# Kernel optimization log

Measured on AMD Instinct MI355X. Metric: run time of the kernel, lower is better.

## Reference

```python
import jax, jax.numpy as jnp
import numpy as np

HEAD_DIM = 128
NUM_HEADS = 16
GROUP_SIZE = 8


def setup_inputs() -> dict:
    key = jax.random.key(0)
    k1, k2, k3 = jax.random.split(key, 3)
    B, T, K = 2, 2048, 2048
    query = jax.random.normal(k1, (B, T, NUM_HEADS * HEAD_DIM), dtype=jnp.float32)
    k_ = jax.random.normal(k2, (B, K, NUM_HEADS, HEAD_DIM), dtype=jnp.float32)
    v_ = jax.random.normal(k3, (B, K, NUM_HEADS, HEAD_DIM), dtype=jnp.float32)
    return {"query": query, "key": k_, "value": v_}


def reference(query, key, value):
    B, T, _ = query.shape
    g = GROUP_SIZE
    # (B, T//g, g, H, D)
    gq = query.reshape(B, T // g, g, NUM_HEADS, HEAD_DIM)
    scale = jnp.sqrt(jnp.asarray(HEAD_DIM, dtype=query.dtype))
    # scores: (B, T//g, g, H, K)
    scores = jnp.einsum('btghd,bkhd->btghk', gq, key) / scale
    attention = jax.nn.softmax(scores, axis=-1)
    out = jnp.einsum('btghk,bkhd->btghd', attention, value)
    return out.reshape(B, T, -1)
```

## Files before the change

kernel.cpp:

```cpp
#include <hip/hip_runtime.h>


#define T_   2048
#define KLEN 2048
#define H_   16
#define D_   128
#define BH_  32
#define NT_  (KLEN / 64)

typedef unsigned short u16;
typedef short bf16x8 __attribute__((ext_vector_type(8), may_alias));
typedef float f32x4 __attribute__((ext_vector_type(4)));
typedef float f32x8 __attribute__((ext_vector_type(8), may_alias));
typedef float f32x16 __attribute__((ext_vector_type(16)));
typedef unsigned int u32a __attribute__((may_alias));
typedef u16 u16a __attribute__((may_alias));

__device__ __forceinline__ u16 f2bf(float f) {
    unsigned int u = __builtin_bit_cast(unsigned int, f);
    u += 0x7fffu + ((u >> 16) & 1u);
    return (u16)(u >> 16);
}
__device__ __forceinline__ unsigned int pk2(float a, float b) {
    unsigned int r;
    asm("v_cvt_pk_bf16_f32 %0, %1, %2" : "=v"(r) : "v"(a), "v"(b));
    return r;
}
__device__ __forceinline__ void pl_swap(unsigned int& a, unsigned int& b) {
    asm("v_permlane32_swap_b32 %0, %1" : "+v"(a), "+v"(b));
}

__device__ __forceinline__ void async_cp16(const void* g, void* l) {
    __builtin_amdgcn_global_load_lds(
        (const __attribute__((address_space(1))) unsigned int*)g,
        (__attribute__((address_space(3))) unsigned int*)l, 16, 0, 0);
}

#define FR_ELEMS ((size_t)KLEN * D_)
#define WS_NEED  (2 * BH_ * FR_ELEMS * sizeof(u16))
#define SM_BUF   32768

__global__ __launch_bounds__(256)
void prep_fused(const float* __restrict__ k_g, const float* __restrict__ v_g,
                u16* __restrict__ kf, u16* __restrict__ vf) {
    __shared__ __align__(16) unsigned char sm[16384];
    if (blockIdx.x < 4096) {
        const int id     = blockIdx.x * 256 + threadIdx.x;
        const int lane   = id & 63;
        const int dchunk = (id >> 6) & 7;
        const int ktile  = (id >> 9) & 1;
        const int kt64   = (id >> 10) & 31;
        const int bh     = id >> 15;
        const int b = bh >> 4, h = bh & 15;
        const int key = kt64 * 64 + ktile * 32 + (lane & 31);
        const int d0  = dchunk * 16 + (lane >> 5) * 8;
        const float* src = k_g + ((size_t)(b * KLEN + key) * H_ + h) * D_ + d0;
        f32x8 v = *(const f32x8*)src;
        uint4 w;
        w.x = pk2(v[0], v[1]); w.y = pk2(v[2], v[3]);
        w.z = pk2(v[4], v[5]); w.w = pk2(v[6], v[7]);
        *(uint4*)(kf + (size_t)id * 8) = w;
    } else {
        const int bid  = blockIdx.x - 4096;
        const int kt64 = bid & 31;
        const int bh   = bid >> 5;
        const int b = bh >> 4, h = bh & 15;
        const float* vbase = v_g + ((size_t)b * KLEN * H_ + h) * D_;
        const int sc0 = threadIdx.x & 15;
        const int spr = threadIdx.x >> 4;
        #pragma unroll
        for (int rr = 0; rr < 2; ++rr) {
            const int r0 = 2 * (spr + 16 * rr);
            const float* vp = vbase + (size_t)(kt64 * 64 + r0) * (H_ * D_) + sc0 * 8;
            f32x8 va = *(const f32x8*)vp;
            f32x8 vb = *(const f32x8*)(vp + H_ * D_);
            const int g_hi = r0 >> 3;
            const int woff = (r0 & 7) * 2;
            #pragma unroll
            for (int j = 0; j < 8; ++j) {
                const int d = sc0 * 8 + j;
                const int g = g_hi ^ ((d ^ (d >> 3)) & 7);
                *(u32a*)(sm + d * 128 + g * 16 + woff) = pk2(va[j], vb[j]);
            }
        }
        __syncthreads();
        u16* obase = vf + (size_t)bh * FR_ELEMS;
        #pragma unroll
        for (int i = 0; i < 4; ++i) {
            const int gid   = threadIdx.x + 256 * i;
            const int lane  = gid & 63;
            const int ntile = (gid >> 6) & 3;
            const int kc    = (gid >> 8) & 3;
            const int key0  = kc * 16 + (lane >> 5) * 8;
            const int d     = ntile * 32 + (lane & 31);
            const int g     = (key0 >> 3) ^ ((d ^ (d >> 3)) & 7);
            uint4 w = *(const uint4*)(sm + d * 128 + g * 16);
            *(uint4*)(obase + ((size_t)(kt64 * 16 + kc * 4 + ntile) * 64 + lane) * 8) = w;
        }
    }
}


struct PA2 { bf16x8 f0, f1; };

__device__ __forceinline__ PA2 softmax_pack(f32x16 st, float kexp, float& lacc) {
    float p[16];
    #pragma unroll
    for (int r = 0; r < 16; ++r) p[r] = exp2f(st[r] * kexp);
    lacc += (((p[0] + p[1]) + (p[2] + p[3])) + ((p[4] + p[5]) + (p[6] + p[7])))
          + (((p[8] + p[9]) + (p[10] + p[11])) + ((p[12] + p[13]) + (p[14] + p[15])));
    unsigned int a0 = pk2(p[0], p[1]),   b0 = pk2(p[4], p[5]);
    unsigned int a1 = pk2(p[2], p[3]),   b1 = pk2(p[6], p[7]);
    unsigned int a2 = pk2(p[8], p[9]),   b2 = pk2(p[12], p[13]);
    unsigned int a3 = pk2(p[10], p[11]), b3 = pk2(p[14], p[15]);
    pl_swap(a0, b0); pl_swap(a1, b1); pl_swap(a2, b2); pl_swap(a3, b3);
    uint4 w0; w0.x = a0; w0.y = a1; w0.z = b0; w0.w = b1;
    uint4 w1; w1.x = a2; w1.y = a3; w1.z = b2; w1.w = b3;
    PA2 r;
    r.f0 = __builtin_bit_cast(bf16x8, w0);
    r.f1 = __builtin_bit_cast(bf16x8, w1);
    return r;
}

__global__ __launch_bounds__(512, 2)
void gqa_fa5(const float* __restrict__ q_g, const u16* __restrict__ kf,
             const u16* __restrict__ vf, float* __restrict__ o_g) {
    __shared__ __align__(16) unsigned char smem[2 * SM_BUF];

    const int lane = threadIdx.x & 63;
    const int wave = threadIdx.x >> 6;
    const int half = lane >> 5;
    const int col  = lane & 31;

    const int blk = blockIdx.x;
    const int bh  = (blk & 7) * 4 + (blk >> 6);
    const int qt  = (blk >> 3) & 7;
    const int b = bh >> 4, h = bh & 15;

    const int q0 = qt * 256 + wave * 32;

    bf16x8 qf[8];
    {
        const float* qbase = q_g + (size_t)(b * T_ + q0 + col) * (H_ * D_)
                                 + h * D_ + half * 8;
        #pragma unroll
        for (int dchunk = 0; dchunk < 8; ++dchunk) {
            f32x8 qv = *(const f32x8*)(qbase + dchunk * 16);
            uint4 w;
            w.x = pk2(qv[0], qv[1]); w.y = pk2(qv[2], qv[3]);
            w.z = pk2(qv[4], qv[5]); w.w = pk2(qv[6], qv[7]);
            qf[dchunk] = __builtin_bit_cast(bf16x8, w);
        }
    }

    const u16* KFb = kf + (size_t)bh * FR_ELEMS;
    const u16* VFb = vf + (size_t)bh * FR_ELEMS;

    f32x16 acc[4] = {};
    float l_part = 0.f;

    const float kexp = 0.12751744f;

    auto stage = [&](int buf, int kt) {
        const u16* ksrc = KFb + (size_t)kt * 8192;
        const u16* vsrc = VFb + (size_t)kt * 8192;
        unsigned char* base = smem + buf * SM_BUF;
        #pragma unroll
        for (int j = 0; j < 4; ++j) {
            const int idx = wave * 4 + j;
            if (idx < 16)
                async_cp16(ksrc + idx * 512 + lane * 8, base + idx * 1024);
            else
                async_cp16(vsrc + (idx - 16) * 512 + lane * 8,
                           base + 16384 + (idx - 16) * 1024);
        }
    };

    stage(0, 0);
    __syncthreads();

    for (int kt = 0; kt < NT_; ++kt) {
        const int cur = kt & 1;
        if (kt + 1 < NT_) stage(cur ^ 1, kt + 1);

        const unsigned char* kbuf = smem + cur * SM_BUF;
        const unsigned char* vbuf = kbuf + 16384;

        f32x16 s0 = {}, s1 = {};
        __builtin_amdgcn_s_setprio(1);
        #pragma unroll
        for (int dchunk = 0; dchunk < 8; ++dchunk) {
            bf16x8 kfr0 = *(const bf16x8*)(kbuf + dchunk * 1024 + lane * 16);
            bf16x8 kfr1 = *(const bf16x8*)(kbuf + (8 + dchunk) * 1024 + lane * 16);
            s0 = __builtin_amdgcn_mfma_f32_32x32x16_bf16(kfr0, qf[dchunk], s0, 0, 0, 0);
            s1 = __builtin_amdgcn_mfma_f32_32x32x16_bf16(kfr1, qf[dchunk], s1, 0, 0, 0);
        }
        __builtin_amdgcn_s_setprio(0);

        PA2 pa01 = softmax_pack(s0, kexp, l_part);
        PA2 pa23 = softmax_pack(s1, kexp, l_part);

        bf16x8 pfrag0 = pa01.f0, pfrag1 = pa01.f1;
        bf16x8 pfrag2 = pa23.f0, pfrag3 = pa23.f1;
        __builtin_amdgcn_s_setprio(1);
        #pragma unroll
        for (int kc = 0; kc < 4; ++kc) {
            const bf16x8 paf = (kc == 0) ? pfrag0 : (kc == 1) ? pfrag1
                             : (kc == 2) ? pfrag2 : pfrag3;
            #pragma unroll
            for (int nt2 = 0; nt2 < 4; ++nt2) {
                bf16x8 vfr = *(const bf16x8*)(vbuf + (kc * 4 + nt2) * 1024 + lane * 16);
                acc[nt2] = __builtin_amdgcn_mfma_f32_32x32x16_bf16(paf, vfr, acc[nt2], 0, 0, 0);
            }
        }
        __builtin_amdgcn_s_setprio(0);

        __syncthreads();
    }

    const float l_full = l_part + __shfl_xor(l_part, 32);
    float* lds_l = (float*)smem;
    if (half == 0) lds_l[wave * 32 + col] = 1.f / l_full;
    __syncthreads();
    #pragma unroll
    for (int r = 0; r < 16; ++r) {
        const int qrow = (r & 3) + 8 * (r >> 2) + 4 * half;
        const float inv = lds_l[wave * 32 + qrow];
        float* op = o_g + (size_t)(b * T_ + q0 + qrow) * (H_ * D_) + h * D_ + col;
        #pragma unroll
        for (int nt2 = 0; nt2 < 4; ++nt2)
            op[nt2 * 32] = acc[nt2][r] * inv;
    }
}


#define VT_BYTES 16384
#define KT_BYTES (64 * 136 * 2)
#define PWF_BYTES 2304

__global__ __launch_bounds__(256, 2)
void gqa_fa_v1(const float* __restrict__ q_g, const float* __restrict__ k_g,
               const float* __restrict__ v_g, float* __restrict__ o_g) {
    __shared__ __align__(16) unsigned char smem[VT_BYTES + KT_BYTES + 4 * PWF_BYTES];
    unsigned char* VtB = smem;
    unsigned char* KtB = smem + VT_BYTES;
    const int lane = threadIdx.x & 63;
    const int wave = threadIdx.x >> 6;
    const int c    = lane & 15;
    const int quad = lane >> 4;
    const int qt = blockIdx.x & 31;
    const int bh = blockIdx.x >> 5;
    const int h  = bh & 15;
    const int b  = bh >> 4;
    const int q0 = qt * 64 + wave * 16;
    bf16x8 qf[4];
    {
        const float* qbase = q_g + (size_t)(b * T_ + q0 + c) * (H_ * D_) + h * D_ + quad * 8;
        #pragma unroll
        for (int dc = 0; dc < 4; ++dc) {
            f32x8 qv = *(const f32x8*)(qbase + dc * 32);
            uint4 w;
            w.x = pk2(qv[0], qv[1]); w.y = pk2(qv[2], qv[3]);
            w.z = pk2(qv[4], qv[5]); w.w = pk2(qv[6], qv[7]);
            qf[dc] = __builtin_bit_cast(bf16x8, w);
        }
    }
    f32x4 acc_o[8];
    #pragma unroll
    for (int dt = 0; dt < 8; ++dt) acc_o[dt] = (f32x4){0.f, 0.f, 0.f, 0.f};
    float m_i[4], l_i[4];
    #pragma unroll
    for (int r = 0; r < 4; ++r) { m_i[r] = -1e30f; l_i[r] = 0.f; }
    const float kexp = 0.12751744f;
    unsigned char* Pw = smem + VT_BYTES + KT_BYTES + wave * PWF_BYTES;
    const int sc0 = threadIdx.x & 15;
    const int spr = threadIdx.x >> 4;
    const size_t kvstride = (size_t)(H_ * D_);
    const float* kbase = k_g + ((size_t)b * KLEN * H_ + h) * D_;
    const float* vbase = v_g + ((size_t)b * KLEN * H_ + h) * D_;
    for (int kt = 0; kt < KLEN / 64; ++kt) {
        __syncthreads();
        #pragma unroll
        for (int i = 0; i < 4; ++i) {
            const int id   = threadIdx.x + 256 * i;
            const int row  = id >> 4;
            const int dcol = (id & 15) * 8;
            const float* kp = kbase + (size_t)(kt * 64 + row) * kvstride + dcol;
            f32x8 kv = *(const f32x8*)kp;
            uint4 w;
            w.x = pk2(kv[0], kv[1]); w.y = pk2(kv[2], kv[3]);
            w.z = pk2(kv[4], kv[5]); w.w = pk2(kv[6], kv[7]);
            *(uint4*)(KtB + (row * 136 + dcol) * 2) = w;
        }
        #pragma unroll
        for (int rr = 0; rr < 2; ++rr) {
            const int r0 = 2 * (spr + 16 * rr);
            const float* vp = vbase + (size_t)(kt * 64 + r0) * kvstride + sc0 * 8;
            f32x8 va = *(const f32x8*)vp;
            f32x8 vb = *(const f32x8*)(vp + kvstride);
            const int g_hi = r0 >> 3;
            const int woff = (r0 & 7) * 2;
            #pragma unroll
            for (int j = 0; j < 8; ++j) {
                const int d = sc0 * 8 + j;
                const int g = g_hi ^ ((d ^ (d >> 3)) & 7);
                *(u32a*)(VtB + d * 128 + g * 16 + woff) = pk2(va[j], vb[j]);
            }
        }
        __syncthreads();
        f32x4 s[4];
        #pragma unroll
        for (int nt = 0; nt < 4; ++nt) {
            s[nt] = (f32x4){0.f, 0.f, 0.f, 0.f};
            const u16* kfp = (const u16*)KtB + (nt * 16 + c) * 136 + quad * 8;
            #pragma unroll
            for (int dc = 0; dc < 4; ++dc) {
                bf16x8 kfr = *(const bf16x8*)(kfp + dc * 32);
                s[nt] = __builtin_amdgcn_mfma_f32_16x16x32_bf16(qf[dc], kfr, s[nt], 0, 0, 0);
            }
        }
        #pragma unroll
        for (int r = 0; r < 4; ++r) {
            float v = fmaxf(fmaxf(s[0][r], s[1][r]), fmaxf(s[2][r], s[3][r]));
            v = fmaxf(v, __shfl_xor(v, 1));
            v = fmaxf(v, __shfl_xor(v, 2));
            v = fmaxf(v, __shfl_xor(v, 4));
            v = fmaxf(v, __shfl_xor(v, 8));
            const float mnew  = fmaxf(m_i[r], v);
            const float alpha = exp2f((m_i[r] - mnew) * kexp);
            m_i[r] = mnew;
            l_i[r] *= alpha;
            #pragma unroll
            for (int dt = 0; dt < 8; ++dt) acc_o[dt][r] *= alpha;
            float sum = 0.f;
            #pragma unroll
            for (int nt = 0; nt < 4; ++nt) {
                const float p = exp2f((s[nt][r] - mnew) * kexp);
                sum += p;
                *(u16a*)(Pw + ((quad * 4 + r) * 72 + nt * 16 + c) * 2) = f2bf(p);
            }
            float t = sum;
            t += __shfl_xor(t, 1);
            t += __shfl_xor(t, 2);
            t += __shfl_xor(t, 4);
            t += __shfl_xor(t, 8);
            l_i[r] += t;
        }
        __syncthreads();
        #pragma unroll
        for (int kc = 0; kc < 2; ++kc) {
            bf16x8 pf = *(const bf16x8*)(Pw + (c * 72 + kc * 32 + quad * 8) * 2);
            const int k0 = kc * 32 + quad * 8;
            #pragma unroll
            for (int dt = 0; dt < 8; ++dt) {
                const int d = dt * 16 + c;
                const int g = (k0 >> 3) ^ ((d ^ (d >> 3)) & 7);
                bf16x8 vfr = *(const bf16x8*)(VtB + d * 128 + g * 16);
                acc_o[dt] = __builtin_amdgcn_mfma_f32_16x16x32_bf16(pf, vfr, acc_o[dt], 0, 0, 0);
            }
        }
    }
    #pragma unroll
    for (int r = 0; r < 4; ++r) {
        const float inv = 1.f / l_i[r];
        const int qrow = q0 + quad * 4 + r;
        float* op = o_g + (size_t)(b * T_ + qrow) * (H_ * D_) + h * D_ + c;
        #pragma unroll
        for (int dt = 0; dt < 8; ++dt)
            op[dt * 16] = acc_o[dt][r] * inv;
    }
}

extern "C" void kernel_launch(void* const* d_in, const int* in_sizes, int n_in,
                              void* d_out, int out_size, void* d_ws, size_t ws_size,
                              hipStream_t stream) {
    const float* q = (const float*)d_in[0];
    const float* k = (const float*)d_in[1];
    const float* v = (const float*)d_in[2];
    float* o = (float*)d_out;
    if (ws_size >= WS_NEED) {
        u16* kfb = (u16*)d_ws;
        u16* vfb = kfb + (size_t)BH_ * FR_ELEMS;
        prep_fused<<<dim3(5120), dim3(256), 0, stream>>>(k, v, kfb, vfb);
        gqa_fa5<<<dim3(256), dim3(512), 0, stream>>>(q, kfb, vfb, o);
    } else {
        gqa_fa_v1<<<dim3(1024), dim3(256), 0, stream>>>(q, k, v, o);
    }
}
```

Before: 206.1 us.

## Stage K conversion through swizzled LDS in same block as V

The prep kernel now handles K and V for the same (bh, 64-key tile) in one block. K rows are read contiguously, converted to bf16, and written to a swizzled LDS buffer, then read back in fragment order for coalesced stores. This replaces the earlier scattered per-thread K gathers and cuts the grid from 5120 to 1024 blocks. The cost is twice the LDS per block and an extra barrier before the K writes.

```diff
diff --git a/kernel.cpp b/kernel.cpp
--- a/kernel.cpp
+++ b/kernel.cpp
@@ -43,31 +43,31 @@
 __global__ __launch_bounds__(256)
 void prep_fused(const float* __restrict__ k_g, const float* __restrict__ v_g,
                 u16* __restrict__ kf, u16* __restrict__ vf) {
-    __shared__ __align__(16) unsigned char sm[16384];
-    if (blockIdx.x < 4096) {
-        const int id     = blockIdx.x * 256 + threadIdx.x;
-        const int lane   = id & 63;
-        const int dchunk = (id >> 6) & 7;
-        const int ktile  = (id >> 9) & 1;
-        const int kt64   = (id >> 10) & 31;
-        const int bh     = id >> 15;
-        const int b = bh >> 4, h = bh & 15;
-        const int key = kt64 * 64 + ktile * 32 + (lane & 31);
-        const int d0  = dchunk * 16 + (lane >> 5) * 8;
-        const float* src = k_g + ((size_t)(b * KLEN + key) * H_ + h) * D_ + d0;
-        f32x8 v = *(const f32x8*)src;
-        uint4 w;
-        w.x = pk2(v[0], v[1]); w.y = pk2(v[2], v[3]);
-        w.z = pk2(v[4], v[5]); w.w = pk2(v[6], v[7]);
-        *(uint4*)(kf + (size_t)id * 8) = w;
-    } else {
-        const int bid  = blockIdx.x - 4096;
-        const int kt64 = bid & 31;
-        const int bh   = bid >> 5;
-        const int b = bh >> 4, h = bh & 15;
+    __shared__ __align__(16) unsigned char smk[16384];
+    __shared__ __align__(16) unsigned char smv[16384];
+    const int kt64 = blockIdx.x & 31;
+    const int bh   = blockIdx.x >> 5;
+    const int b = bh >> 4, h = bh & 15;
+    const int tid = threadIdx.x;
+
+    {
+        const float* kbase = k_g + ((size_t)(b * KLEN + kt64 * 64) * H_ + h) * D_;
+        #pragma unroll
+        for (int i = 0; i < 4; ++i) {
+            const int gid  = tid + 256 * i;
+            const int row  = gid >> 4;
+            const int col8 = gid & 15;
+            f32x8 kv = *(const f32x8*)(kbase + (size_t)row * (H_ * D_) + col8 * 8);
+            uint4 w;
+            w.x = pk2(kv[0], kv[1]); w.y = pk2(kv[2], kv[3]);
+            w.z = pk2(kv[4], kv[5]); w.w = pk2(kv[6], kv[7]);
+            *(uint4*)(smk + row * 256 + ((col8 ^ (row & 15)) * 16)) = w;
+        }
+    }
+    {
         const float* vbase = v_g + ((size_t)b * KLEN * H_ + h) * D_;
-        const int sc0 = threadIdx.x & 15;
-        const int spr = threadIdx.x >> 4;
+        const int sc0 = tid & 15;
+        const int spr = tid >> 4;
         #pragma unroll
         for (int rr = 0; rr < 2; ++rr) {
             const int r0 = 2 * (spr + 16 * rr);
@@ -80,21 +80,37 @@
             for (int j = 0; j < 8; ++j) {
                 const int d = sc0 * 8 + j;
                 const int g = g_hi ^ ((d ^ (d >> 3)) & 7);
-                *(u32a*)(sm + d * 128 + g * 16 + woff) = pk2(va[j], vb[j]);
-            }
-        }
-        __syncthreads();
+                *(u32a*)(smv + d * 128 + g * 16 + woff) = pk2(va[j], vb[j]);
+            }
+        }
+    }
+    __syncthreads();
+    {
+        u16* obase = kf + (size_t)bh * FR_ELEMS + (size_t)kt64 * 8192;
+        #pragma unroll
+        for (int i = 0; i < 4; ++i) {
+            const int gid    = tid + 256 * i;
+            const int lane   = gid & 63;
+            const int dchunk = (gid >> 6) & 7;
+            const int ktile  = gid >> 9;
+            const int key  = ktile * 32 + (lane & 31);
+            const int col8 = dchunk * 2 + (lane >> 5);
+            uint4 w = *(const uint4*)(smk + key * 256 + ((col8 ^ (key & 15)) * 16));
+            *(uint4*)(obase + (size_t)gid * 8) = w;
+        }
+    }
+    {
         u16* obase = vf + (size_t)bh * FR_ELEMS;
         #pragma unroll
         for (int i = 0; i < 4; ++i) {
-            const int gid   = threadIdx.x + 256 * i;
+            const int gid   = tid + 256 * i;
             const int lane  = gid & 63;
             const int ntile = (gid >> 6) & 3;
             const int kc    = (gid >> 8) & 3;
             const int key0  = kc * 16 + (lane >> 5) * 8;
             const int d     = ntile * 32 + (lane & 31);
             const int g     = (key0 >> 3) ^ ((d ^ (d >> 3)) & 7);
-            uint4 w = *(const uint4*)(sm + d * 128 + g * 16);
+            uint4 w = *(const uint4*)(smv + d * 128 + g * 16);
             *(uint4*)(obase + ((size_t)(kt64 * 16 + kc * 4 + ntile) * 64 + lane) * 8) = w;
         }
     }
@@ -381,7 +397,7 @@
     if (ws_size >= WS_NEED) {
         u16* kfb = (u16*)d_ws;
         u16* vfb = kfb + (size_t)BH_ * FR_ELEMS;
-        prep_fused<<<dim3(5120), dim3(256), 0, stream>>>(k, v, kfb, vfb);
+        prep_fused<<<dim3(1024), dim3(256), 0, stream>>>(k, v, kfb, vfb);
         gqa_fa5<<<dim3(256), dim3(512), 0, stream>>>(q, kfb, vfb, o);
     } else {
         gqa_fa_v1<<<dim3(1024), dim3(256), 0, stream>>>(q, k, v, o);
```

Measured after the change: 206.0 us. No clear change (-0.1%).
